# Kernel tuning notes

Measured on AMD Instinct MI355X. Metric: run time of the kernel, lower is better.

## Reference

```python
import jax, jax.numpy as jnp
import numpy as np

B, N, K, F, OUT = 32, 2000, 32, 64, 128

def setup_inputs() -> dict:
    key = jax.random.key(0)
    k1, k2, k3, k4, k5 = jax.random.split(key, 5)
    x = jax.random.normal(k1, (B, N, F), dtype=jnp.float32)
    neighborhood = jax.random.randint(k2, (N, K), 0, N, dtype=jnp.int64)
    distances = jax.random.uniform(k3, (N, K), dtype=jnp.float32)
    # Linear(k*(F+1), OUT): torch default init scale ~ 1/sqrt(fan_in)
    fan_in = K * (F + 1)
    W = jax.random.normal(k4, (OUT, fan_in), dtype=jnp.float32) / np.sqrt(fan_in)
    b = jax.random.normal(k5, (OUT,), dtype=jnp.float32) / np.sqrt(fan_in)
    return {"x": x, "neighborhood": neighborhood, "distances": distances, "W": W, "b": b}

def reference(x, neighborhood, distances, W, b):
    batch, seq_len, feat = x.shape          # [B, N, F]
    k = neighborhood.shape[1]
    gathered = x[:, neighborhood, :]        # [B, N, K, F] gather over sequence dim
    d = jnp.broadcast_to(distances[None, :, :, None], (batch, seq_len, k, 1))
    h = jnp.concatenate([gathered, d], axis=-1)        # [B, N, K, F+1]
    h = h.reshape(batch, seq_len, k * (feat + 1))      # [B, N, K*(F+1)]
    out = jnp.einsum('bnf,of->bno', h, W) + b          # [B, N, OUT]
    return out
```

## Files before the change

### kernel.cpp

```cpp
#include <hip/hip_runtime.h>
#include <hip/hip_bf16.h>
#include <stdint.h>

typedef __attribute__((ext_vector_type(8)))  __bf16   bf16x8;
typedef __attribute__((ext_vector_type(16))) float    f32x16;
typedef __attribute__((ext_vector_type(8)))  float    f32x8;

#define NB   32
#define NN   2000
#define NK   32
#define NF   64
#define NOUT 128
#define NSTEP 130

#define GLOBAL_AS __attribute__((address_space(1)))
#define LDS_AS    __attribute__((address_space(3)))
#define SB() __builtin_amdgcn_sched_barrier(0)

__global__ void kprep(const float* __restrict__ x, const float* __restrict__ dist,
                      const float* __restrict__ W,
                      __bf16* __restrict__ xb2, __bf16* __restrict__ db,
                      __bf16* __restrict__ Wf) {
  const int t = threadIdx.x;
  if (blockIdx.x < NN) {
    __shared__ __bf16 sm[32 * 66];
    const int n = blockIdx.x;
    const int bb = t >> 3;
    const int f0 = (t & 7) << 3;
    const float* src = x + ((size_t)bb * NN + n) * NF + f0;
    f32x8 v = *(const f32x8*)src;
    bf16x8 r;
#pragma unroll
    for (int j = 0; j < 8; ++j) r[j] = (__bf16)v[j];
    *(bf16x8*)&sm[bb * 66 + f0] = r;
    __syncthreads();
    const int col = t & 31, half = (t >> 5) & 1, s = t >> 6;
    bf16x8 o = *(const bf16x8*)&sm[col * 66 + s * 16 + half * 8];
    *(bf16x8*)((char*)xb2 + ((size_t)n << 12) + t * 16) = o;
    if (t < NK) db[n * NK + t] = (__bf16)dist[n * NK + t];
  } else {
    const int kstep = blockIdx.x - NN;
    const int lane = t & 63;
    const int wv = t >> 6;
    const int o = wv * 32 + (lane & 31);
    const int kbase = kstep * 16 + (lane >> 5) * 8;
    bf16x8 r;
#pragma unroll
    for (int j = 0; j < 8; ++j) {
      const int kg = kbase + j;
      const int c = (kg < 2048) ? ((kg >> 6) * 65 + (kg & 63)) : ((kg - 2048) * 65 + 64);
      r[j] = (__bf16)W[(size_t)o * 2080 + c];
    }
    *(bf16x8*)(Wf + (((size_t)kstep * 256 + t) << 3)) = r;
  }
}

__global__ __launch_bounds__(256, 2) void kmain(
    const int* __restrict__ nbrs, const float* __restrict__ bias,
    const __bf16* __restrict__ xb2, const __bf16* __restrict__ Wf,
    const __bf16* __restrict__ db, float* __restrict__ out) {
  __shared__ __align__(16) char lds[2][8][4096];

  const int t    = threadIdx.x;
  const int lane = t & 63;
  const int w    = t >> 6;
  const int nh   = w >> 1;
  const int ogp  = w & 1;
  const int col  = lane & 31;
  const int half = lane >> 5;
  const int n0   = blockIdx.x * 4;
  const int q    = nh * 2 + ogp;

  f32x16 acc00 = {}, acc01 = {}, acc10 = {}, acc11 = {};

  int myidx = 0;
  if (lane < NK) myidx = nbrs[(n0 + q) * NK + lane];

  const char* wfb = (const char*)Wf + (ogp << 11) + lane * 16;

  auto stage = [&](int buf, int sc) {
#pragma unroll
    for (int p = 0; p < 2; ++p) {
      const int nb = __builtin_amdgcn_readlane(myidx, sc * 2 + p);
      const char* g = (const char*)xb2 + ((size_t)nb << 12) + lane * 16;
      char* l = &lds[buf][q * 2 + p][0];
#pragma unroll
      for (int qq = 0; qq < 4; ++qq)
        __builtin_amdgcn_global_load_lds(
            (const GLOBAL_AS uint32_t*)(g + (qq << 10)),
            (LDS_AS uint32_t*)(l + (qq << 10)), 16, 0, 0);
    }
  };

  auto loadB = [&](bf16x8* B, int sc) {
    const char* base = wfb + ((size_t)sc << 15);
#pragma unroll
    for (int ps = 0; ps < 8; ++ps) {
      B[ps * 2 + 0] = *(const bf16x8*)(base + (ps << 12));
      B[ps * 2 + 1] = *(const bf16x8*)(base + (ps << 12) + 1024);
    }
  };

  auto compute = [&](int buf, const bf16x8* B) {
    __builtin_amdgcn_s_setprio(1);
#pragma unroll
    for (int p = 0; p < 2; ++p) {
#pragma unroll
      for (int s = 0; s < 4; ++s) {
        const char* la = &lds[buf][(nh * 2 + 0) * 2 + p][0] + (s << 10) + lane * 16;
        const char* lb = &lds[buf][(nh * 2 + 1) * 2 + p][0] + (s << 10) + lane * 16;
        bf16x8 a0 = *(const bf16x8*)(la);
        bf16x8 a1 = *(const bf16x8*)(lb);
        const int ps = p * 4 + s;
        acc00 = __builtin_amdgcn_mfma_f32_32x32x16_bf16(a0, B[ps * 2 + 0], acc00, 0, 0, 0);
        acc01 = __builtin_amdgcn_mfma_f32_32x32x16_bf16(a0, B[ps * 2 + 1], acc01, 0, 0, 0);
        acc10 = __builtin_amdgcn_mfma_f32_32x32x16_bf16(a1, B[ps * 2 + 0], acc10, 0, 0, 0);
        acc11 = __builtin_amdgcn_mfma_f32_32x32x16_bf16(a1, B[ps * 2 + 1], acc11, 0, 0, 0);
      }
    }
    __builtin_amdgcn_s_setprio(0);
  };

  bf16x8 BA[16], BB[16];

  stage(0, 0); SB();
  loadB(BA, 0); SB();

#define PERIOD(SC, BC, BL)                                   \
  loadB(BL, (SC) + 1); SB();                                 \
  asm volatile("s_waitcnt vmcnt(16)" ::: "memory");          \
  __builtin_amdgcn_s_barrier(); SB();                        \
  stage(((SC) + 1) & 1, (SC) + 1); SB();                     \
  compute((SC) & 1, BC);

  for (int sc = 0; sc < 14; sc += 2) {
    PERIOD(sc + 0, BA, BB)
    PERIOD(sc + 1, BB, BA)
  }
#undef PERIOD
  loadB(BB, 15); SB();
  asm volatile("s_waitcnt vmcnt(16)" ::: "memory");
  __builtin_amdgcn_s_barrier(); SB();
  stage(1, 15); SB();
  compute(0, BA);
  asm volatile("s_waitcnt vmcnt(0)" ::: "memory");
  __builtin_amdgcn_s_barrier(); SB();
  compute(1, BB);

#pragma unroll
  for (int s = 0; s < 2; ++s) {
    const char* wt = wfb + ((size_t)(128 + s) << 12);
    bf16x8 b0 = *(const bf16x8*)(wt);
    bf16x8 b1 = *(const bf16x8*)(wt + 1024);
    const char* dbase = (const char*)db + (size_t)(n0 + nh * 2) * 64 + s * 32 + half * 16;
    bf16x8 d0 = *(const bf16x8*)(dbase);
    bf16x8 d1 = *(const bf16x8*)(dbase + 64);
    acc00 = __builtin_amdgcn_mfma_f32_32x32x16_bf16(d0, b0, acc00, 0, 0, 0);
    acc01 = __builtin_amdgcn_mfma_f32_32x32x16_bf16(d0, b1, acc01, 0, 0, 0);
    acc10 = __builtin_amdgcn_mfma_f32_32x32x16_bf16(d1, b0, acc10, 0, 0, 0);
    acc11 = __builtin_amdgcn_mfma_f32_32x32x16_bf16(d1, b1, acc11, 0, 0, 0);
  }

  const int o0 = (ogp << 6) + col;
  const int nn = n0 + nh * 2;
  const float bv0 = bias[o0], bv1 = bias[o0 + 32];
#pragma unroll
  for (int r = 0; r < 16; ++r) {
    const int row = (r & 3) + 8 * (r >> 2) + 4 * half;
    float* op = out + ((size_t)row * NN + nn) * NOUT + o0;
    op[0]         = acc00[r] + bv0;
    op[32]        = acc01[r] + bv1;
    op[NOUT]      = acc10[r] + bv0;
    op[NOUT + 32] = acc11[r] + bv1;
  }
}

extern "C" void kernel_launch(void* const* d_in, const int* in_sizes, int n_in,
                              void* d_out, int out_size, void* d_ws, size_t ws_size,
                              hipStream_t stream) {
  const float* x    = (const float*)d_in[0];
  const int*   nbrs = (const int*)d_in[1];
  const float* dist = (const float*)d_in[2];
  const float* W    = (const float*)d_in[3];
  const float* bias = (const float*)d_in[4];
  float* out = (float*)d_out;

  char* ws = (char*)d_ws;
  __bf16* xb2 = (__bf16*)(ws);
  __bf16* Wf  = (__bf16*)(ws + 8192000);
  __bf16* db  = (__bf16*)(ws + 8192000 + 532480);

  kprep<<<NN + NSTEP, 256, 0, stream>>>(x, dist, W, xb2, db, Wf);
  kmain<<<NN / 4, 256, 0, stream>>>(nbrs, bias, xb2, Wf, db, out);
}
```

Before: 58.83 us.

## Swap operand staging: keep gathered x in registers, share W via LDS

Each wave now owns one sequence position and all 128 outputs. It loads its gathered neighbor rows straight into registers, while the weight slice for each step is staged once per block into double-buffered LDS with async global-to-LDS loads and shared by all four waves. Before, each wave kept two node rows and half the outputs and loaded its weight slice into registers itself. The aim is to cut duplicated weight fetches from global memory and balance register use. In exchange, every MFMA now reads its B operand from LDS, and gathered rows are no longer shared between waves.

```diff
diff --git a/kernel.cpp b/kernel.cpp
--- a/kernel.cpp
+++ b/kernel.cpp
@@ -16,6 +16,7 @@
 #define GLOBAL_AS __attribute__((address_space(1)))
 #define LDS_AS    __attribute__((address_space(3)))
 #define SB() __builtin_amdgcn_sched_barrier(0)
+#define MFMA __builtin_amdgcn_mfma_f32_32x32x16_bf16
 
 __global__ void kprep(const float* __restrict__ x, const float* __restrict__ dist,
                       const float* __restrict__ W,
@@ -59,119 +60,108 @@
     const int* __restrict__ nbrs, const float* __restrict__ bias,
     const __bf16* __restrict__ xb2, const __bf16* __restrict__ Wf,
     const __bf16* __restrict__ db, float* __restrict__ out) {
-  __shared__ __align__(16) char lds[2][8][4096];
+  __shared__ __align__(16) char lds[2][32768];
 
   const int t    = threadIdx.x;
   const int lane = t & 63;
   const int w    = t >> 6;
-  const int nh   = w >> 1;
-  const int ogp  = w & 1;
   const int col  = lane & 31;
   const int half = lane >> 5;
   const int n0   = blockIdx.x * 4;
-  const int q    = nh * 2 + ogp;
+  const int n    = n0 + w;
 
-  f32x16 acc00 = {}, acc01 = {}, acc10 = {}, acc11 = {};
+  f32x16 acc0 = {}, acc1 = {}, acc2 = {}, acc3 = {};
 
   int myidx = 0;
-  if (lane < NK) myidx = nbrs[(n0 + q) * NK + lane];
+  if (lane < NK) myidx = nbrs[n * NK + lane];
 
-  const char* wfb = (const char*)Wf + (ogp << 11) + lane * 16;
-
-  auto stage = [&](int buf, int sc) {
+  auto loadA = [&](bf16x8* A, int c) {
 #pragma unroll
     for (int p = 0; p < 2; ++p) {
-      const int nb = __builtin_amdgcn_readlane(myidx, sc * 2 + p);
+      const int nb = __builtin_amdgcn_readlane(myidx, c * 2 + p);
       const char* g = (const char*)xb2 + ((size_t)nb << 12) + lane * 16;
-      char* l = &lds[buf][q * 2 + p][0];
 #pragma unroll
-      for (int qq = 0; qq < 4; ++qq)
-        __builtin_amdgcn_global_load_lds(
-            (const GLOBAL_AS uint32_t*)(g + (qq << 10)),
-            (LDS_AS uint32_t*)(l + (qq << 10)), 16, 0, 0);
+      for (int s = 0; s < 4; ++s)
+        A[p * 4 + s] = *(const bf16x8*)(g + (s << 10));
     }
   };
 
-  auto loadB = [&](bf16x8* B, int sc) {
-    const char* base = wfb + ((size_t)sc << 15);
+  auto stageB = [&](int c) {
+    const char* g = (const char*)Wf + ((size_t)c << 15) + (w << 10) + lane * 16;
+    char* l = &lds[c & 1][w << 10];
 #pragma unroll
-    for (int ps = 0; ps < 8; ++ps) {
-      B[ps * 2 + 0] = *(const bf16x8*)(base + (ps << 12));
-      B[ps * 2 + 1] = *(const bf16x8*)(base + (ps << 12) + 1024);
-    }
+    for (int q = 0; q < 8; ++q)
+      __builtin_amdgcn_global_load_lds(
+          (const GLOBAL_AS uint32_t*)(g + (q << 12)),
+          (LDS_AS uint32_t*)(l + (q << 12)), 16, 0, 0);
   };
 
-  auto compute = [&](int buf, const bf16x8* B) {
+  auto compute = [&](int c, const bf16x8* A) {
+    const char* lb = &lds[c & 1][0] + lane * 16;
     __builtin_amdgcn_s_setprio(1);
 #pragma unroll
-    for (int p = 0; p < 2; ++p) {
-#pragma unroll
-      for (int s = 0; s < 4; ++s) {
-        const char* la = &lds[buf][(nh * 2 + 0) * 2 + p][0] + (s << 10) + lane * 16;
-        const char* lb = &lds[buf][(nh * 2 + 1) * 2 + p][0] + (s << 10) + lane * 16;
-        bf16x8 a0 = *(const bf16x8*)(la);
-        bf16x8 a1 = *(const bf16x8*)(lb);
-        const int ps = p * 4 + s;
-        acc00 = __builtin_amdgcn_mfma_f32_32x32x16_bf16(a0, B[ps * 2 + 0], acc00, 0, 0, 0);
-        acc01 = __builtin_amdgcn_mfma_f32_32x32x16_bf16(a0, B[ps * 2 + 1], acc01, 0, 0, 0);
-        acc10 = __builtin_amdgcn_mfma_f32_32x32x16_bf16(a1, B[ps * 2 + 0], acc10, 0, 0, 0);
-        acc11 = __builtin_amdgcn_mfma_f32_32x32x16_bf16(a1, B[ps * 2 + 1], acc11, 0, 0, 0);
-      }
+    for (int ks = 0; ks < 8; ++ks) {
+      bf16x8 b0 = *(const bf16x8*)(lb + (ks << 12));
+      bf16x8 b1 = *(const bf16x8*)(lb + (ks << 12) + 1024);
+      bf16x8 b2 = *(const bf16x8*)(lb + (ks << 12) + 2048);
+      bf16x8 b3 = *(const bf16x8*)(lb + (ks << 12) + 3072);
+      acc0 = MFMA(A[ks], b0, acc0, 0, 0, 0);
+      acc1 = MFMA(A[ks], b1, acc1, 0, 0, 0);
+      acc2 = MFMA(A[ks], b2, acc2, 0, 0, 0);
+      acc3 = MFMA(A[ks], b3, acc3, 0, 0, 0);
     }
     __builtin_amdgcn_s_setprio(0);
   };
 
-  bf16x8 BA[16], BB[16];
+  bf16x8 AA[8], AB[8];
 
-  stage(0, 0); SB();
-  loadB(BA, 0); SB();
+  loadA(AA, 0); SB();
+  stageB(0); SB();
 
-#define PERIOD(SC, BC, BL)                                   \
-  loadB(BL, (SC) + 1); SB();                                 \
-  asm volatile("s_waitcnt vmcnt(16)" ::: "memory");          \
-  __builtin_amdgcn_s_barrier(); SB();                        \
-  stage(((SC) + 1) & 1, (SC) + 1); SB();                     \
-  compute((SC) & 1, BC);
+#define BODY(C, AC, AL)                                     \
+  loadA(AL, (C) + 1); SB();                                 \
+  asm volatile("s_waitcnt vmcnt(8)" ::: "memory");          \
+  __builtin_amdgcn_s_barrier(); SB();                       \
+  compute((C), AC); SB();                                   \
+  stageB((C) + 1); SB();
 
-  for (int sc = 0; sc < 14; sc += 2) {
-    PERIOD(sc + 0, BA, BB)
-    PERIOD(sc + 1, BB, BA)
+  for (int c = 0; c < 14; c += 2) {
+    BODY(c + 0, AA, AB)
+    BODY(c + 1, AB, AA)
   }
-#undef PERIOD
-  loadB(BB, 15); SB();
-  asm volatile("s_waitcnt vmcnt(16)" ::: "memory");
+#undef BODY
+  loadA(AB, 15); SB();
+  asm volatile("s_waitcnt vmcnt(8)" ::: "memory");
   __builtin_amdgcn_s_barrier(); SB();
-  stage(1, 15); SB();
-  compute(0, BA);
+  compute(14, AA); SB();
+  stageB(15); SB();
   asm volatile("s_waitcnt vmcnt(0)" ::: "memory");
   __builtin_amdgcn_s_barrier(); SB();
-  compute(1, BB);
+  compute(15, AB);
 
 #pragma unroll
   for (int s = 0; s < 2; ++s) {
-    const char* wt = wfb + ((size_t)(128 + s) << 12);
+    const char* wt = (const char*)Wf + ((size_t)(128 + s) << 12) + lane * 16;
+    bf16x8 dv = *(const bf16x8*)((const char*)db + (size_t)n * 64 + s * 32 + half * 16);
     bf16x8 b0 = *(const bf16x8*)(wt);
     bf16x8 b1 = *(const bf16x8*)(wt + 1024);
-    const char* dbase = (const char*)db + (size_t)(n0 + nh * 2) * 64 + s * 32 + half * 16;
-    bf16x8 d0 = *(const bf16x8*)(dbase);
-    bf16x8 d1 = *(const bf16x8*)(dbase + 64);
-    acc00 = __builtin_amdgcn_mfma_f32_32x32x16_bf16(d0, b0, acc00, 0, 0, 0);
-    acc01 = __builtin_amdgcn_mfma_f32_32x32x16_bf16(d0, b1, acc01, 0, 0, 0);
-    acc10 = __builtin_amdgcn_mfma_f32_32x32x16_bf16(d1, b0, acc10, 0, 0, 0);
-    acc11 = __builtin_amdgcn_mfma_f32_32x32x16_bf16(d1, b1, acc11, 0, 0, 0);
+    bf16x8 b2 = *(const bf16x8*)(wt + 2048);
+    bf16x8 b3 = *(const bf16x8*)(wt + 3072);
+    acc0 = MFMA(dv, b0, acc0, 0, 0, 0);
+    acc1 = MFMA(dv, b1, acc1, 0, 0, 0);
+    acc2 = MFMA(dv, b2, acc2, 0, 0, 0);
+    acc3 = MFMA(dv, b3, acc3, 0, 0, 0);
   }
 
-  const int o0 = (ogp << 6) + col;
-  const int nn = n0 + nh * 2;
-  const float bv0 = bias[o0], bv1 = bias[o0 + 32];
+  const float bv0 = bias[col], bv1 = bias[col + 32], bv2 = bias[col + 64], bv3 = bias[col + 96];
 #pragma unroll
   for (int r = 0; r < 16; ++r) {
     const int row = (r & 3) + 8 * (r >> 2) + 4 * half;
-    float* op = out + ((size_t)row * NN + nn) * NOUT + o0;
-    op[0]         = acc00[r] + bv0;
-    op[32]        = acc01[r] + bv1;
-    op[NOUT]      = acc10[r] + bv0;
-    op[NOUT + 32] = acc11[r] + bv1;
+    float* op = out + ((size_t)row * NN + n) * NOUT + col;
+    op[0]  = acc0[r] + bv0;
+    op[32] = acc1[r] + bv1;
+    op[64] = acc2[r] + bv2;
+    op[96] = acc3[r] + bv3;
   }
 }
 
```

Result: faster. 54.93 us (-6.6%).
